# Kernel tuning notes

Measured on AMD Instinct MI355X. Metric: run time of the kernel, lower is better.

The kernel has to match this reference:

```python
import jax, jax.numpy as jnp
import numpy as np

N = 100000
IN_DIM = 128
HID = 64
OUT = 4


def _gcn_conv(x, W, b, src, dst, deg_inv_sqrt):
    """PyG GCNConv: linear transform, then symmetric-normalized scatter-add.
    src/dst already include self-loops; deg_inv_sqrt precomputed over them."""
    h = x @ W                                   # [N, H]
    norm = deg_inv_sqrt[src] * deg_inv_sqrt[dst]  # [E+N]
    msg = h[src] * norm[:, None]                # gather + scale, [E+N, H]
    out = jax.ops.segment_sum(msg, dst, num_segments=N)  # scatter-add
    return out + b


def setup_inputs() -> dict:
    key = jax.random.key(0)
    ks = jax.random.split(key, 8)
    E = 1600000
    x = jax.random.normal(ks[0], (N, IN_DIM), dtype=jnp.float32)
    edge_index = jax.random.randint(ks[1], (2, E), 0, N, dtype=jnp.int32)
    # Glorot-ish init for weights
    W1 = jax.random.normal(ks[2], (IN_DIM, HID), dtype=jnp.float32) / np.sqrt(IN_DIM)
    b1 = jnp.zeros((HID,), dtype=jnp.float32)
    W2 = jax.random.normal(ks[3], (HID, HID), dtype=jnp.float32) / np.sqrt(HID)
    b2 = jnp.zeros((HID,), dtype=jnp.float32)
    Wfc = jax.random.normal(ks[4], (HID, OUT), dtype=jnp.float32) / np.sqrt(HID)
    bfc = jnp.zeros((OUT,), dtype=jnp.float32)
    return {"x": x, "edge_index": edge_index, "W1": W1, "b1": b1,
            "W2": W2, "b2": b2, "Wfc": Wfc, "bfc": bfc}


def reference(x, edge_index, W1, b1, W2, b2, Wfc, bfc):
    # Add self-loops (GCNConv default add_self_loops=True)
    loops = jnp.arange(N, dtype=edge_index.dtype)
    src = jnp.concatenate([edge_index[0], loops])
    dst = jnp.concatenate([edge_index[1], loops])
    # Symmetric normalization: deg computed at aggregation targets (dst)
    deg = jax.ops.segment_sum(jnp.ones_like(dst, dtype=x.dtype), dst,
                              num_segments=N)
    deg_inv_sqrt = jnp.where(deg > 0, jax.lax.rsqrt(deg), 0.0)

    h = _gcn_conv(x, W1, b1, src, dst, deg_inv_sqrt)
    h = jax.nn.relu(h)                 # dropout is identity in eval mode
    h = _gcn_conv(h, W2, b2, src, dst, deg_inv_sqrt)
    h = jax.nn.relu(h)
    return h @ Wfc + bfc               # [N, 4]
```

## Files before the change

### kernel.cpp

```cpp
#include <hip/hip_runtime.h>
#include <hip/hip_fp16.h>


#define BCAP 5120
#define BINB 512
#define CHUNK 3200

typedef float v2f __attribute__((ext_vector_type(2)));
typedef _Float16 f16x8 __attribute__((ext_vector_type(8)));
typedef float f32x4 __attribute__((ext_vector_type(4)));

__global__ __launch_bounds__(256) void k_prep(const float* __restrict__ W1,
                                              const float* __restrict__ W2,
                                              _Float16* __restrict__ wt1,
                                              _Float16* __restrict__ wt2,
                                              int* __restrict__ bcur) {
    int gid = threadIdx.x + blockIdx.x * blockDim.x;
    {
        int k = gid >> 6, nn = gid & 63;
        wt1[nn * 136 + k] = (_Float16)W1[gid];
    }
    if (gid < 64 * 64) {
        int k = gid >> 6, nn = gid & 63;
        wt2[nn * 72 + k] = (_Float16)W2[gid];
    }
    if (gid < 512) bcur[gid] = 0;
}

__global__ __launch_bounds__(256) void k_bin(const int* __restrict__ src,
                                             const int* __restrict__ dst, int e,
                                             int* bcur, unsigned* __restrict__ binned) {
    __shared__ unsigned ec[CHUNK];
    __shared__ unsigned short eb[CHUNK];
    __shared__ int lh[512], lbase[512], lr[512];
    int t = threadIdx.x;
    for (int i = t; i < 512; i += 256) { lh[i] = 0; lr[i] = 0; }
    __syncthreads();
    int chunk = (e + gridDim.x - 1) / gridDim.x;
    int lo = blockIdx.x * chunk;
    int hi = min(e, lo + chunk);
    for (int i = lo + t; i < hi; i += 256) {
        int d = dst[i];
        int b = d >> 8;
        ec[i - lo] = ((unsigned)src[i] << 8) | (unsigned)(d & 255);
        eb[i - lo] = (unsigned short)b;
        atomicAdd(&lh[b], 1);
    }
    __syncthreads();
    for (int i = t; i < 512; i += 256)
        lbase[i] = lh[i] ? atomicAdd(&bcur[i], lh[i]) : 0;
    __syncthreads();
    int cnt = hi - lo;
    for (int i = t; i < cnt; i += 256) {
        int b = eb[i];
        int r = lbase[b] + atomicAdd(&lr[b], 1);
        if (r < BCAP)
            binned[(size_t)b * BCAP + r] = ec[i];
    }
}

__global__ __launch_bounds__(256) void k_bucket(const unsigned* __restrict__ binned,
                                                const int* __restrict__ bcur,
                                                int n, int* __restrict__ offs,
                                                int* __restrict__ cnt,
                                                float* __restrict__ dis,
                                                int* __restrict__ csr) {
    __shared__ unsigned ec[BCAP];
    __shared__ int nh[256], nsc[256], nr[256];
    int b = blockIdx.x, t = threadIdx.x;
    int node0 = b << 8;
    size_t ebase = (size_t)b * BCAP;
    int ecnt = min(bcur[b], BCAP);
    nh[t] = 0; nr[t] = 0;
    __syncthreads();
    for (int j = t; j < ecnt; j += 256) {
        unsigned ed = binned[ebase + j];
        ec[j] = ed;
        atomicAdd(&nh[ed & 255u], 1);
    }
    __syncthreads();
    int v = nh[t];
    nsc[t] = v;
    __syncthreads();
    for (int o = 1; o < 256; o <<= 1) {
        int x = (t >= o) ? nsc[t - o] : 0;
        __syncthreads();
        nsc[t] += x;
        __syncthreads();
    }
    int ex = nsc[t] - v;
    int d = node0 + t;
    if (d < n) {
        offs[d] = (int)ebase + ex;
        cnt[d]  = v;
        dis[d]  = rsqrtf((float)(v + 1));
    }
    nsc[t] = ex;
    __syncthreads();
    for (int j = t; j < ecnt; j += 256) {
        unsigned ed = ec[j];
        int ld = ed & 255u;
        int r = atomicAdd(&nr[ld], 1);
        csr[ebase + nsc[ld] + r] = (int)(ed >> 8);
    }
}

template<int K, typename TI>
__global__ __launch_bounds__(256) void k_gemm_mfma(const TI* __restrict__ X,
                                                   const _Float16* __restrict__ Wt,
                                                   const float* __restrict__ dis,
                                                   __half* __restrict__ Hh, int n) {
    constexpr int KP = K + 8;
    __shared__ _Float16 As[128 * KP];
    __shared__ _Float16 Bs[64 * KP];

    int t = threadIdx.x;
    _Float16* H = (_Float16*)Hh;

    constexpr int NF4 = 64 * KP / 8;
    for (int i = t; i < NF4; i += 256)
        ((float4*)Bs)[i] = ((const float4*)Wt)[i];

    int row0 = blockIdx.x * 128;
    if (sizeof(TI) == 4) {
        const float* Xf = (const float*)X;
        #pragma unroll
        for (int p = 0; p < 8; ++p) {
            int gi  = t + p * 256;
            int row = gi >> 4, sg = gi & 15;
            int grow = row0 + row;
            float4 v0 = make_float4(0.f, 0.f, 0.f, 0.f), v1 = v0;
            if (grow < n) {
                v0 = *(const float4*)(Xf + (size_t)grow * K + sg * 8);
                v1 = *(const float4*)(Xf + (size_t)grow * K + sg * 8 + 4);
            }
            union { __half2 h[4]; float4 f; } u;
            u.h[0] = __floats2half2_rn(v0.x, v0.y);
            u.h[1] = __floats2half2_rn(v0.z, v0.w);
            u.h[2] = __floats2half2_rn(v1.x, v1.y);
            u.h[3] = __floats2half2_rn(v1.z, v1.w);
            *(float4*)(As + row * KP + sg * 8) = u.f;
        }
    } else {
        const __half* Xh = (const __half*)X;
        #pragma unroll
        for (int p = 0; p < 4; ++p) {
            int gi  = t + p * 256;
            int row = gi >> 3, sg = gi & 7;
            int grow = row0 + row;
            float4 v = make_float4(0.f, 0.f, 0.f, 0.f);
            if (grow < n)
                v = *(const float4*)(Xh + (size_t)grow * K + sg * 8);
            *(float4*)(As + row * KP + sg * 8) = v;
        }
    }
    __syncthreads();

    int wv   = t >> 6;
    int lane = t & 63;
    int m    = lane & 15;
    int quad = lane >> 4;
    int r0   = wv * 32;

    f32x4 acc[2][4] = {};
    #pragma unroll
    for (int kb = 0; kb < K / 32; ++kb) {
        f16x8 af0 = *(const f16x8*)(As + (r0 + m) * KP + quad * 8 + kb * 32);
        f16x8 af1 = *(const f16x8*)(As + (r0 + 16 + m) * KP + quad * 8 + kb * 32);
        #pragma unroll
        for (int nt = 0; nt < 4; ++nt) {
            f16x8 bf = *(const f16x8*)(Bs + (nt * 16 + m) * KP + quad * 8 + kb * 32);
            acc[0][nt] = __builtin_amdgcn_mfma_f32_16x16x32_f16(af0, bf, acc[0][nt], 0, 0, 0);
            acc[1][nt] = __builtin_amdgcn_mfma_f32_16x16x32_f16(af1, bf, acc[1][nt], 0, 0, 0);
        }
    }

    #pragma unroll
    for (int mt = 0; mt < 2; ++mt) {
        float dv[4]; int gr[4];
        #pragma unroll
        for (int r = 0; r < 4; ++r) {
            gr[r] = row0 + r0 + mt * 16 + quad * 4 + r;
            dv[r] = (gr[r] < n) ? dis[gr[r]] : 0.f;
        }
        #pragma unroll
        for (int nt = 0; nt < 4; ++nt)
            #pragma unroll
            for (int r = 0; r < 4; ++r) {
                if (gr[r] < n)
                    H[(size_t)gr[r] * 64 + nt * 16 + m] =
                        (_Float16)(acc[mt][nt][r] * dv[r]);
                else if (gr[r] == n)
                    H[(size_t)n * 64 + nt * 16 + m] = (_Float16)0.f;
            }
    }
}

__device__ inline void add_row(const __half* __restrict__ hp, int s, int c4,
                               v2f& lo, v2f& hi) {
    float2 raw = *(const float2*)(hp + (size_t)s * 64 + c4);
    const __half2* p = (const __half2*)&raw;
    float2 l = __half22float2(p[0]);
    float2 h = __half22float2(p[1]);
    lo += (v2f){ l.x, l.y };
    hi += (v2f){ h.x, h.y };
}

template<bool FUSE>
__global__ __launch_bounds__(256) void k_gather(const __half* __restrict__ hp,
                                                const int* __restrict__ csr,
                                                const int* __restrict__ off,
                                                const int* __restrict__ cnt,
                                                const float* __restrict__ dis,
                                                const float* __restrict__ bias,
                                                void* __restrict__ outb,
                                                const float* __restrict__ Wfc,
                                                const float* __restrict__ bfc,
                                                int n) {
    int lane = threadIdx.x & 63;
    int wid  = (blockIdx.x * blockDim.x + threadIdx.x) >> 6;
    if (wid >= n) return;
    int d    = wid;
    int esub = lane >> 4;
    int c4   = (lane & 15) * 4;

    int start = off[d], num = cnt[d];
    int idx = (lane < num) ? csr[start + lane] : 0;
    int lim = min(num, 64);

    v2f aL[4] = {}, aH[4] = {};
    if (esub == 0)
        add_row(hp, d, c4, aL[0], aH[0]);

    int j = 0;
    for (; j + 16 <= lim; j += 16) {
        int s0 = __shfl(idx, j + esub);
        int s1 = __shfl(idx, j + 4 + esub);
        int s2 = __shfl(idx, j + 8 + esub);
        int s3 = __shfl(idx, j + 12 + esub);
        add_row(hp, s0, c4, aL[0], aH[0]);
        add_row(hp, s1, c4, aL[1], aH[1]);
        add_row(hp, s2, c4, aL[2], aH[2]);
        add_row(hp, s3, c4, aL[3], aH[3]);
    }
    for (; j < lim; j += 4) {
        int jj = j + esub;
        int sr = __shfl(idx, jj);
        int s  = (jj < lim) ? sr : n;
        add_row(hp, s, c4, aL[0], aH[0]);
    }
    for (int j2 = 64; j2 < num; j2 += 4) {
        int jj = j2 + esub;
        if (jj < num) {
            int s = csr[start + jj];
            add_row(hp, s, c4, aL[1], aH[1]);
        }
    }
    v2f sL = (aL[0] + aL[1]) + (aL[2] + aL[3]);
    v2f sH = (aH[0] + aH[1]) + (aH[2] + aH[3]);
    float4 a0 = make_float4(sL.x, sL.y, sH.x, sH.y);
    #pragma unroll
    for (int o = 16; o <= 32; o <<= 1) {
        a0.x += __shfl_xor(a0.x, o);
        a0.y += __shfl_xor(a0.y, o);
        a0.z += __shfl_xor(a0.z, o);
        a0.w += __shfl_xor(a0.w, o);
    }
    float dd = dis[d];
    float4 bb = *(const float4*)(bias + c4);
    float4 o;
    o.x = fmaxf(bb.x + dd * a0.x, 0.f);
    o.y = fmaxf(bb.y + dd * a0.y, 0.f);
    o.z = fmaxf(bb.z + dd * a0.z, 0.f);
    o.w = fmaxf(bb.w + dd * a0.w, 0.f);
    if (!FUSE) {
        if (esub == 0) {
            union { __half2 h[2]; float2 f; } u;
            u.h[0] = __floats2half2_rn(o.x, o.y);
            u.h[1] = __floats2half2_rn(o.z, o.w);
            *(float2*)((__half*)outb + (size_t)d * 64 + c4) = u.f;
        }
    } else {
        const float4* W4 = (const float4*)Wfc;
        float4 w0 = W4[c4 + 0], w1 = W4[c4 + 1], w2 = W4[c4 + 2], w3 = W4[c4 + 3];
        float4 p;
        p.x = o.x * w0.x + o.y * w1.x + o.z * w2.x + o.w * w3.x;
        p.y = o.x * w0.y + o.y * w1.y + o.z * w2.y + o.w * w3.y;
        p.z = o.x * w0.z + o.y * w1.z + o.z * w2.z + o.w * w3.z;
        p.w = o.x * w0.w + o.y * w1.w + o.z * w2.w + o.w * w3.w;
        #pragma unroll
        for (int q = 1; q <= 8; q <<= 1) {
            p.x += __shfl_xor(p.x, q);
            p.y += __shfl_xor(p.y, q);
            p.z += __shfl_xor(p.z, q);
            p.w += __shfl_xor(p.w, q);
        }
        if (lane == 0) {
            float4 bf = *(const float4*)bfc;
            float4 r = make_float4(p.x + bf.x, p.y + bf.y, p.z + bf.z, p.w + bf.w);
            ((float4*)outb)[d] = r;
        }
    }
}

static inline size_t align256(size_t x) { return (x + 255) & ~(size_t)255; }

extern "C" void kernel_launch(void* const* d_in, const int* in_sizes, int n_in,
                              void* d_out, int out_size, void* d_ws, size_t ws_size,
                              hipStream_t stream) {
    const float* x   = (const float*)d_in[0];
    const int*   ei  = (const int*)d_in[1];
    const float* W1  = (const float*)d_in[2];
    const float* b1  = (const float*)d_in[3];
    const float* W2  = (const float*)d_in[4];
    const float* b2  = (const float*)d_in[5];
    const float* Wfc = (const float*)d_in[6];
    const float* bfc = (const float*)d_in[7];
    float* out = (float*)d_out;

    int n = in_sizes[0] / 128;
    int e = in_sizes[1] / 2;
    const int* src = ei;
    const int* dst = ei + e;

    char* ws = (char*)d_ws;
    size_t p = 0;
    float*    dis    = (float*)   (ws + p); p = align256(p + (size_t)n * 4);
    int*      counts = (int*)     (ws + p); p = align256(p + (size_t)n * 4);
    int*      offs   = (int*)     (ws + p); p = align256(p + (size_t)n * 4);
    int*      bcur   = (int*)     (ws + p); p = align256(p + 512 * 4);
    _Float16* wt1    = (_Float16*)(ws + p); p = align256(p + 64 * 136 * 2);
    _Float16* wt2    = (_Float16*)(ws + p); p = align256(p + 64 * 72 * 2);
    int*      csr    = (int*)     (ws + p); p = align256(p + (size_t)512 * BCAP * 4);
    unsigned* binned = (unsigned*)(ws + p); p = align256(p + (size_t)512 * BCAP * 4);
    __half*   hbuf   = (__half*)  (ws + p); p = align256(p + (size_t)(n + 1) * 64 * 2);
    __half*   a1h    = (__half*)  (ws + p);

    int gb  = (n + 127) / 128;
    int nbk = (n + 255) / 256;

    k_prep<<<32, 256, 0, stream>>>(W1, W2, wt1, wt2, bcur);
    k_bin<<<BINB, 256, 0, stream>>>(src, dst, e, bcur, binned);
    k_bucket<<<nbk, 256, 0, stream>>>(binned, bcur, n, offs, counts, dis, csr);

    k_gemm_mfma<128, float><<<gb, 256, 0, stream>>>(x, wt1, dis, hbuf, n);
    k_gather<false><<<(n * 64 + 255) / 256, 256, 0, stream>>>(
        hbuf, csr, offs, counts, dis, b1, a1h, nullptr, nullptr, n);

    k_gemm_mfma<64, __half><<<gb, 256, 0, stream>>>(a1h, wt2, dis, hbuf, n);
    k_gather<true><<<(n * 64 + 255) / 256, 256, 0, stream>>>(
        hbuf, csr, offs, counts, dis, b2, out, Wfc, bfc, n);
}
```

Measured before the change: 264.3 us.

## Fuse edge binning with first GEMM and move source normalization into gather

```diff
diff --git a/kernel.cpp b/kernel.cpp
--- a/kernel.cpp
+++ b/kernel.cpp
@@ -10,52 +10,125 @@
 typedef _Float16 f16x8 __attribute__((ext_vector_type(8)));
 typedef float f32x4 __attribute__((ext_vector_type(4)));
 
-__global__ __launch_bounds__(256) void k_prep(const float* __restrict__ W1,
-                                              const float* __restrict__ W2,
-                                              _Float16* __restrict__ wt1,
-                                              _Float16* __restrict__ wt2,
-                                              int* __restrict__ bcur) {
-    int gid = threadIdx.x + blockIdx.x * blockDim.x;
-    {
-        int k = gid >> 6, nn = gid & 63;
-        wt1[nn * 136 + k] = (_Float16)W1[gid];
-    }
-    if (gid < 64 * 64) {
-        int k = gid >> 6, nn = gid & 63;
-        wt2[nn * 72 + k] = (_Float16)W2[gid];
-    }
-    if (gid < 512) bcur[gid] = 0;
-}
-
-__global__ __launch_bounds__(256) void k_bin(const int* __restrict__ src,
-                                             const int* __restrict__ dst, int e,
-                                             int* bcur, unsigned* __restrict__ binned) {
-    __shared__ unsigned ec[CHUNK];
-    __shared__ unsigned short eb[CHUNK];
-    __shared__ int lh[512], lbase[512], lr[512];
+__global__ __launch_bounds__(256) void k_bin_gemm1(
+        const int* __restrict__ src, const int* __restrict__ dst, int e,
+        int* bcur, unsigned* __restrict__ binned,
+        const float* __restrict__ X, const float* __restrict__ W1,
+        __half* __restrict__ Hh, int n) {
+    __shared__ union {
+        struct {
+            unsigned ec[CHUNK];
+            unsigned short eb[CHUNK];
+            int lh[512], lbase[512], lr[512];
+        } b;
+        struct {
+            _Float16 As[128 * 136];
+            _Float16 Bs[64 * 136];
+        } g;
+    } sm;
+
     int t = threadIdx.x;
-    for (int i = t; i < 512; i += 256) { lh[i] = 0; lr[i] = 0; }
-    __syncthreads();
-    int chunk = (e + gridDim.x - 1) / gridDim.x;
-    int lo = blockIdx.x * chunk;
-    int hi = min(e, lo + chunk);
-    for (int i = lo + t; i < hi; i += 256) {
-        int d = dst[i];
-        int b = d >> 8;
-        ec[i - lo] = ((unsigned)src[i] << 8) | (unsigned)(d & 255);
-        eb[i - lo] = (unsigned short)b;
-        atomicAdd(&lh[b], 1);
-    }
-    __syncthreads();
-    for (int i = t; i < 512; i += 256)
-        lbase[i] = lh[i] ? atomicAdd(&bcur[i], lh[i]) : 0;
-    __syncthreads();
-    int cnt = hi - lo;
-    for (int i = t; i < cnt; i += 256) {
-        int b = eb[i];
-        int r = lbase[b] + atomicAdd(&lr[b], 1);
-        if (r < BCAP)
-            binned[(size_t)b * BCAP + r] = ec[i];
+
+    if (blockIdx.x < BINB) {
+        unsigned* ec = sm.b.ec;
+        unsigned short* eb = sm.b.eb;
+        int* lh = sm.b.lh; int* lbase = sm.b.lbase; int* lr = sm.b.lr;
+        for (int i = t; i < 512; i += 256) { lh[i] = 0; lr[i] = 0; }
+        __syncthreads();
+        int chunk = (e + BINB - 1) / BINB;
+        int lo = blockIdx.x * chunk;
+        int hi = min(e, lo + chunk);
+        for (int i = lo + t; i < hi; i += 256) {
+            int d = dst[i];
+            int b = d >> 8;
+            ec[i - lo] = ((unsigned)src[i] << 8) | (unsigned)(d & 255);
+            eb[i - lo] = (unsigned short)b;
+            atomicAdd(&lh[b], 1);
+        }
+        __syncthreads();
+        for (int i = t; i < 512; i += 256)
+            lbase[i] = lh[i] ? atomicAdd(&bcur[i], lh[i]) : 0;
+        __syncthreads();
+        int cnt = hi - lo;
+        for (int i = t; i < cnt; i += 256) {
+            int b = eb[i];
+            int r = lbase[b] + atomicAdd(&lr[b], 1);
+            if (r < BCAP)
+                binned[(size_t)b * BCAP + r] = ec[i];
+        }
+    } else {
+        constexpr int K = 128, KP = 136;
+        _Float16* As = sm.g.As;
+        _Float16* Bs = sm.g.Bs;
+        _Float16* H = (_Float16*)Hh;
+
+        #pragma unroll
+        for (int p = 0; p < 8; ++p) {
+            int i = t + p * 256;
+            int k = i >> 4, nn4 = (i & 15) << 2;
+            float4 v = ((const float4*)W1)[i];
+            Bs[(nn4 + 0) * KP + k] = (_Float16)v.x;
+            Bs[(nn4 + 1) * KP + k] = (_Float16)v.y;
+            Bs[(nn4 + 2) * KP + k] = (_Float16)v.z;
+            Bs[(nn4 + 3) * KP + k] = (_Float16)v.w;
+        }
+
+        int row0 = (blockIdx.x - BINB) * 128;
+        #pragma unroll
+        for (int p = 0; p < 8; ++p) {
+            int gi  = t + p * 256;
+            int row = gi >> 4, sg = gi & 15;
+            int grow = row0 + row;
+            float4 v0 = make_float4(0.f, 0.f, 0.f, 0.f), v1 = v0;
+            if (grow < n) {
+                v0 = *(const float4*)(X + (size_t)grow * K + sg * 8);
+                v1 = *(const float4*)(X + (size_t)grow * K + sg * 8 + 4);
+            }
+            union { __half2 h[4]; float4 f; } u;
+            u.h[0] = __floats2half2_rn(v0.x, v0.y);
+            u.h[1] = __floats2half2_rn(v0.z, v0.w);
+            u.h[2] = __floats2half2_rn(v1.x, v1.y);
+            u.h[3] = __floats2half2_rn(v1.z, v1.w);
+            *(float4*)(As + row * KP + sg * 8) = u.f;
+        }
+        __syncthreads();
+
+        int wv   = t >> 6;
+        int lane = t & 63;
+        int m    = lane & 15;
+        int quad = lane >> 4;
+        int r0   = wv * 32;
+
+        f32x4 acc[2][4] = {};
+        #pragma unroll
+        for (int kb = 0; kb < K / 32; ++kb) {
+            f16x8 af0 = *(const f16x8*)(As + (r0 + m) * KP + quad * 8 + kb * 32);
+            f16x8 af1 = *(const f16x8*)(As + (r0 + 16 + m) * KP + quad * 8 + kb * 32);
+            #pragma unroll
+            for (int nt = 0; nt < 4; ++nt) {
+                f16x8 bf = *(const f16x8*)(Bs + (nt * 16 + m) * KP + quad * 8 + kb * 32);
+                acc[0][nt] = __builtin_amdgcn_mfma_f32_16x16x32_f16(af0, bf, acc[0][nt], 0, 0, 0);
+                acc[1][nt] = __builtin_amdgcn_mfma_f32_16x16x32_f16(af1, bf, acc[1][nt], 0, 0, 0);
+            }
+        }
+
+        #pragma unroll
+        for (int mt = 0; mt < 2; ++mt) {
+            int gr[4];
+            #pragma unroll
+            for (int r = 0; r < 4; ++r)
+                gr[r] = row0 + r0 + mt * 16 + quad * 4 + r;
+            #pragma unroll
+            for (int nt = 0; nt < 4; ++nt)
+                #pragma unroll
+                for (int r = 0; r < 4; ++r) {
+                    if (gr[r] < n)
+                        H[(size_t)gr[r] * 64 + nt * 16 + m] =
+                            (_Float16)acc[mt][nt][r];
+                    else if (gr[r] == n)
+                        H[(size_t)n * 64 + nt * 16 + m] = (_Float16)0.f;
+                }
+        }
     }
 }
 
@@ -105,54 +178,39 @@
     }
 }
 
-template<int K, typename TI>
-__global__ __launch_bounds__(256) void k_gemm_mfma(const TI* __restrict__ X,
-                                                   const _Float16* __restrict__ Wt,
-                                                   const float* __restrict__ dis,
-                                                   __half* __restrict__ Hh, int n) {
-    constexpr int KP = K + 8;
+__global__ __launch_bounds__(256) void k_gemm2(const __half* __restrict__ X,
+                                               const float* __restrict__ W2,
+                                               const float* __restrict__ dis,
+                                               __half* __restrict__ Hh, int n) {
+    constexpr int K = 64, KP = 72;
     __shared__ _Float16 As[128 * KP];
     __shared__ _Float16 Bs[64 * KP];
 
     int t = threadIdx.x;
     _Float16* H = (_Float16*)Hh;
 
-    constexpr int NF4 = 64 * KP / 8;
-    for (int i = t; i < NF4; i += 256)
-        ((float4*)Bs)[i] = ((const float4*)Wt)[i];
+    #pragma unroll
+    for (int p = 0; p < 4; ++p) {
+        int i = t + p * 256;
+        int k = i >> 4, nn4 = (i & 15) << 2;
+        float4 v = ((const float4*)W2)[i];
+        Bs[(nn4 + 0) * KP + k] = (_Float16)v.x;
+        Bs[(nn4 + 1) * KP + k] = (_Float16)v.y;
+        Bs[(nn4 + 2) * KP + k] = (_Float16)v.z;
+        Bs[(nn4 + 3) * KP + k] = (_Float16)v.w;
+    }
 
     int row0 = blockIdx.x * 128;
-    if (sizeof(TI) == 4) {
-        const float* Xf = (const float*)X;
-        #pragma unroll
-        for (int p = 0; p < 8; ++p) {
-            int gi  = t + p * 256;
-            int row = gi >> 4, sg = gi & 15;
-            int grow = row0 + row;
-            float4 v0 = make_float4(0.f, 0.f, 0.f, 0.f), v1 = v0;
-            if (grow < n) {
-                v0 = *(const float4*)(Xf + (size_t)grow * K + sg * 8);
-                v1 = *(const float4*)(Xf + (size_t)grow * K + sg * 8 + 4);
-            }
-            union { __half2 h[4]; float4 f; } u;
-            u.h[0] = __floats2half2_rn(v0.x, v0.y);
-            u.h[1] = __floats2half2_rn(v0.z, v0.w);
-            u.h[2] = __floats2half2_rn(v1.x, v1.y);
-            u.h[3] = __floats2half2_rn(v1.z, v1.w);
-            *(float4*)(As + row * KP + sg * 8) = u.f;
-        }
-    } else {
-        const __half* Xh = (const __half*)X;
-        #pragma unroll
-        for (int p = 0; p < 4; ++p) {
-            int gi  = t + p * 256;
-            int row = gi >> 3, sg = gi & 7;
-            int grow = row0 + row;
-            float4 v = make_float4(0.f, 0.f, 0.f, 0.f);
-            if (grow < n)
-                v = *(const float4*)(Xh + (size_t)grow * K + sg * 8);
-            *(float4*)(As + row * KP + sg * 8) = v;
-        }
+    const __half* Xh = X;
+    #pragma unroll
+    for (int p = 0; p < 4; ++p) {
+        int gi  = t + p * 256;
+        int row = gi >> 3, sg = gi & 7;
+        int grow = row0 + row;
+        float4 v = make_float4(0.f, 0.f, 0.f, 0.f);
+        if (grow < n)
+            v = *(const float4*)(Xh + (size_t)grow * K + sg * 8);
+        *(float4*)(As + row * KP + sg * 8) = v;
     }
     __syncthreads();
 
@@ -206,7 +264,17 @@
     hi += (v2f){ h.x, h.y };
 }
 
-template<bool FUSE>
+__device__ inline void fma_row(const __half* __restrict__ hp, int s, int c4,
+                               float w, v2f& lo, v2f& hi) {
+    float2 raw = *(const float2*)(hp + (size_t)s * 64 + c4);
+    const __half2* p = (const __half2*)&raw;
+    float2 l = __half22float2(p[0]);
+    float2 h = __half22float2(p[1]);
+    lo += w * (v2f){ l.x, l.y };
+    hi += w * (v2f){ h.x, h.y };
+}
+
+template<bool FUSE, bool SCALE>
 __global__ __launch_bounds__(256) void k_gather(const __half* __restrict__ hp,
                                                 const int* __restrict__ csr,
                                                 const int* __restrict__ off,
@@ -226,11 +294,16 @@
 
     int start = off[d], num = cnt[d];
     int idx = (lane < num) ? csr[start + lane] : 0;
+    float dsv = 0.f;
+    if constexpr (SCALE) dsv = dis[idx];
+    float dd = dis[d];
     int lim = min(num, 64);
 
     v2f aL[4] = {}, aH[4] = {};
-    if (esub == 0)
-        add_row(hp, d, c4, aL[0], aH[0]);
+    if (esub == 0) {
+        if constexpr (SCALE) fma_row(hp, d, c4, dd, aL[0], aH[0]);
+        else                 add_row(hp, d, c4, aL[0], aH[0]);
+    }
 
     int j = 0;
     for (; j + 16 <= lim; j += 16) {
@@ -238,22 +311,39 @@
         int s1 = __shfl(idx, j + 4 + esub);
         int s2 = __shfl(idx, j + 8 + esub);
         int s3 = __shfl(idx, j + 12 + esub);
-        add_row(hp, s0, c4, aL[0], aH[0]);
-        add_row(hp, s1, c4, aL[1], aH[1]);
-        add_row(hp, s2, c4, aL[2], aH[2]);
-        add_row(hp, s3, c4, aL[3], aH[3]);
+        if constexpr (SCALE) {
+            float w0 = __shfl(dsv, j + esub);
+            float w1 = __shfl(dsv, j + 4 + esub);
+            float w2 = __shfl(dsv, j + 8 + esub);
+            float w3 = __shfl(dsv, j + 12 + esub);
+            fma_row(hp, s0, c4, w0, aL[0], aH[0]);
+            fma_row(hp, s1, c4, w1, aL[1], aH[1]);
+            fma_row(hp, s2, c4, w2, aL[2], aH[2]);
+            fma_row(hp, s3, c4, w3, aL[3], aH[3]);
+        } else {
+            add_row(hp, s0, c4, aL[0], aH[0]);
+            add_row(hp, s1, c4, aL[1], aH[1]);
+            add_row(hp, s2, c4, aL[2], aH[2]);
+            add_row(hp, s3, c4, aL[3], aH[3]);
+        }
     }
     for (; j < lim; j += 4) {
         int jj = j + esub;
         int sr = __shfl(idx, jj);
         int s  = (jj < lim) ? sr : n;
-        add_row(hp, s, c4, aL[0], aH[0]);
+        if constexpr (SCALE) {
+            float w = __shfl(dsv, jj);
+            fma_row(hp, s, c4, w, aL[0], aH[0]);
+        } else {
+            add_row(hp, s, c4, aL[0], aH[0]);
+        }
     }
     for (int j2 = 64; j2 < num; j2 += 4) {
         int jj = j2 + esub;
         if (jj < num) {
             int s = csr[start + jj];
-            add_row(hp, s, c4, aL[1], aH[1]);
+            if constexpr (SCALE) fma_row(hp, s, c4, dis[s], aL[1], aH[1]);
+            else                 add_row(hp, s, c4, aL[1], aH[1]);
         }
     }
     v2f sL = (aL[0] + aL[1]) + (aL[2] + aL[3]);
@@ -266,7 +356,6 @@
         a0.z += __shfl_xor(a0.z, o);
         a0.w += __shfl_xor(a0.w, o);
     }
-    float dd = dis[d];
     float4 bb = *(const float4*)(bias + c4);
     float4 o;
     o.x = fmaxf(bb.x + dd * a0.x, 0.f);
@@ -329,8 +418,6 @@
     int*      counts = (int*)     (ws + p); p = align256(p + (size_t)n * 4);
     int*      offs   = (int*)     (ws + p); p = align256(p + (size_t)n * 4);
     int*      bcur   = (int*)     (ws + p); p = align256(p + 512 * 4);
-    _Float16* wt1    = (_Float16*)(ws + p); p = align256(p + 64 * 136 * 2);
-    _Float16* wt2    = (_Float16*)(ws + p); p = align256(p + 64 * 72 * 2);
     int*      csr    = (int*)     (ws + p); p = align256(p + (size_t)512 * BCAP * 4);
     unsigned* binned = (unsigned*)(ws + p); p = align256(p + (size_t)512 * BCAP * 4);
     __half*   hbuf   = (__half*)  (ws + p); p = align256(p + (size_t)(n + 1) * 64 * 2);
@@ -339,15 +426,15 @@
     int gb  = (n + 127) / 128;
     int nbk = (n + 255) / 256;
 
-    k_prep<<<32, 256, 0, stream>>>(W1, W2, wt1, wt2, bcur);
-    k_bin<<<BINB, 256, 0, stream>>>(src, dst, e, bcur, binned);
+    hipMemsetAsync(bcur, 0, 512 * sizeof(int), stream);
+    k_bin_gemm1<<<BINB + gb, 256, 0, stream>>>(src, dst, e, bcur, binned,
+                                               x, W1, hbuf, n);
     k_bucket<<<nbk, 256, 0, stream>>>(binned, bcur, n, offs, counts, dis, csr);
 
-    k_gemm_mfma<128, float><<<gb, 256, 0, stream>>>(x, wt1, dis, hbuf, n);
-    k_gather<false><<<(n * 64 + 255) / 256, 256, 0, stream>>>(
+    k_gather<false, true><<<(n * 64 + 255) / 256, 256, 0, stream>>>(
         hbuf, csr, offs, counts, dis, b1, a1h, nullptr, nullptr, n);
 
-    k_gemm_mfma<64, __half><<<gb, 256, 0, stream>>>(a1h, wt2, dis, hbuf, n);
-    k_gather<true><<<(n * 64 + 255) / 256, 256, 0, stream>>>(
+    k_gemm2<<<gb, 256, 0, stream>>>(a1h, W2, dis, hbuf, n);
+    k_gather<true, false><<<(n * 64 + 255) / 256, 256, 0, stream>>>(
         hbuf, csr, offs, counts, dis, b2, out, Wfc, bfc, n);
 }
```

Result: faster. 257.5 us (-2.6%).
